# Optimization experiments

Measured on AMD Instinct MI355X. Metric: run time of the kernel, lower is better.

## Reference

```python
import jax, jax.numpy as jnp
import numpy as np

EMBED_DIM = 1024
NUM_HEADS = 16
HEAD_DIM = EMBED_DIM // NUM_HEADS
SCALE = 1.0 / np.sqrt(HEAD_DIM).astype(np.float32)


def setup_inputs() -> dict:
    key = jax.random.key(0)
    ks = jax.random.split(key, 9)
    B, T, C = 2, 2048, EMBED_DIM
    s = 1.0 / np.sqrt(C).astype(np.float32)  # torch Linear init scale (approx, uniform bound)
    return {
        "x_q": jax.random.normal(ks[0], (B, T, C), dtype=jnp.float32),
        "attn_mask": jnp.zeros((T, T), dtype=jnp.float32),
        "Wq": jax.random.uniform(ks[1], (C, C), jnp.float32, -s, s),
        "bq": jax.random.uniform(ks[2], (C,), jnp.float32, -s, s),
        "Wk": jax.random.uniform(ks[3], (C, C), jnp.float32, -s, s),
        "bk": jax.random.uniform(ks[4], (C,), jnp.float32, -s, s),
        "Wv": jax.random.uniform(ks[5], (C, C), jnp.float32, -s, s),
        "bv": jax.random.uniform(ks[6], (C,), jnp.float32, -s, s),
        "Wo": jax.random.uniform(ks[7], (C, C), jnp.float32, -s, s),
        "bo": jax.random.uniform(ks[8], (C,), jnp.float32, -s, s),
    }


def reference(x_q, attn_mask, Wq, bq, Wk, bk, Wv, bv, Wo, bo):
    B, Tq, C = x_q.shape
    # self-attention: x_kv = x_q
    q = (x_q @ Wq.T + bq).reshape(B, Tq, NUM_HEADS, HEAD_DIM)
    k = (x_q @ Wk.T + bk).reshape(B, Tq, NUM_HEADS, HEAD_DIM)
    v = (x_q @ Wv.T + bv).reshape(B, Tq, NUM_HEADS, HEAD_DIM)
    # (B, H, Tq, Tk)
    scores = jnp.einsum('bqhd,bkhd->bhqk', q, k) * SCALE
    scores = scores + attn_mask[None, None, :, :]  # 2D additive mask path
    attn = jax.nn.softmax(scores, axis=-1)  # dropout p=0.0 -> identity
    out = jnp.einsum('bhqk,bkhd->bqhd', attn, v).reshape(B, Tq, C)
    out = out @ Wo.T + bo
    return out
```

## Files before the change

kernel.cpp:

```cpp
#include <hip/hip_runtime.h>
#include <hip/hip_bf16.h>
#include <stdint.h>

typedef _Float16 f16x8_t __attribute__((ext_vector_type(8)));
typedef _Float16 f16x4_t __attribute__((ext_vector_type(4)));
typedef float    f32x4_t __attribute__((ext_vector_type(4)));

#define T_SEQ 2048
#define NH    16
#define HD    64
#define CDIM  1024
#define NTOK  4096
#define QSCALE 0.18033688011112042f
#define LOG2E  1.4426950408889634f

__device__ __forceinline__ void async_ld16(void* lds, const void* g) {
    __builtin_amdgcn_global_load_lds(
        (const __attribute__((address_space(1))) uint32_t*)g,
        (__attribute__((address_space(3))) uint32_t*)lds, 16, 0, 0);
}

__global__ __launch_bounds__(256)
void prep_all(const float* __restrict__ x, const float* __restrict__ Wq,
              const float* __restrict__ Wk, const float* __restrict__ Wv,
              const float* __restrict__ Wo, const float* __restrict__ mask,
              _Float16* __restrict__ xh, _Float16* __restrict__ Wqkvh,
              _Float16* __restrict__ Woh, int* __restrict__ flag)
{
    const int XQ = NTOK * CDIM / 4;
    const int WQ = CDIM * CDIM / 4;
    int i = blockIdx.x * 256 + threadIdx.x;
    if (i < XQ + 4 * WQ) {
        const float* s; _Float16* d; int off;
        if (i < XQ) { s = x; d = xh; off = i; }
        else {
            int j = i - XQ; int w = j >> 18; off = j & (WQ - 1);
            s = (w == 0) ? Wq : (w == 1) ? Wk : (w == 2) ? Wv : Wo;
            d = (w == 3) ? Woh : Wqkvh + (size_t)w * CDIM * CDIM;
        }
        float4 v = ((const float4*)s)[off];
        f16x4_t h = {(_Float16)v.x, (_Float16)v.y, (_Float16)v.z, (_Float16)v.w};
        ((f16x4_t*)d)[off] = h;
    } else {
        int off = i - (XQ + 4 * WQ);
        float4 v = ((const float4*)mask)[off];
        if (v.x != 0.f || v.y != 0.f || v.z != 0.f || v.w != 0.f) atomicOr(flag, 1);
    }
}

template<int MODE>
__global__ __launch_bounds__(256)
void gemm_f16(const _Float16* __restrict__ Ag, const _Float16* __restrict__ Bg,
              const float* __restrict__ b0, const float* __restrict__ b1,
              const float* __restrict__ b2,
              _Float16* __restrict__ Qo, _Float16* __restrict__ Ko,
              _Float16* __restrict__ Vto, float* __restrict__ Fo)
{
    __shared__ _Float16 sA[2][128 * 32];
    __shared__ _Float16 sB[2][128 * 32];
    const int K = CDIM;
    const int NBX = (MODE == 0) ? 24 : 8;
    const int NWG = NBX * 32;
    const int tid  = threadIdx.x;
    const int lane = tid & 63, wv = tid >> 6;
    const int wr = wv >> 1, wc = wv & 1;
    const int bid = blockIdx.x;
    const int swz = (bid & 7) * (NWG / 8) + (bid >> 3);
    const int rowA0 = (swz % NBX) * 128;
    const int rowB0 = (swz / NBX) * 128;
    const int srow = lane >> 2;
    const int scol = (lane & 3) * 8;
    const int fr = lane & 15, fg = lane >> 4;
    f32x4_t acc[4][4] = {};

#define STAGE(buf, kk) do {                                                     \
        _Pragma("unroll")                                                       \
        for (int i_ = 0; i_ < 2; ++i_) {                                        \
            const int eoff = i_ * 2048 + wv * 512;                              \
            const int r_ = i_ * 64 + wv * 16 + srow;                            \
            async_ld16(&sA[buf][eoff], Ag + (size_t)(rowA0 + r_) * K + (kk) + scol); \
            async_ld16(&sB[buf][eoff], Bg + (size_t)(rowB0 + r_) * K + (kk) + scol); \
        } } while (0)

    STAGE(0, 0);
    for (int k0 = 0; k0 < K; k0 += 32) {
        const int cur = (k0 >> 5) & 1;
        __syncthreads();
        if (k0 + 32 < K) STAGE(cur ^ 1, k0 + 32);
        f16x8_t a[4], b[4];
#pragma unroll
        for (int mi = 0; mi < 4; ++mi)
            a[mi] = *(const f16x8_t*)&sA[cur][(wr * 64 + mi * 16 + fr) * 32 + fg * 8];
#pragma unroll
        for (int ni = 0; ni < 4; ++ni)
            b[ni] = *(const f16x8_t*)&sB[cur][(wc * 64 + ni * 16 + fr) * 32 + fg * 8];
#pragma unroll
        for (int mi = 0; mi < 4; ++mi)
#pragma unroll
            for (int ni = 0; ni < 4; ++ni)
                acc[mi][ni] = __builtin_amdgcn_mfma_f32_16x16x32_f16(a[mi], b[ni], acc[mi][ni], 0, 0, 0);
    }
#undef STAGE

    if (MODE == 0) {
        const int which = rowA0 >> 10;
        const float* bp = (which == 0) ? b0 : ((which == 1) ? b1 : b2);
#pragma unroll
        for (int mi = 0; mi < 4; ++mi) {
            const int cc = (rowA0 & 1023) + wr * 64 + mi * 16 + fg * 4;
            const float4 bv = *(const float4*)&bp[cc];
            const int h = cc >> 6, d0 = cc & 63;
#pragma unroll
            for (int ni = 0; ni < 4; ++ni) {
                const int tok = rowB0 + wc * 64 + ni * 16 + fr;
                const int bh = (tok >> 11) * NH + h, tt = tok & (T_SEQ - 1);
                const float v0 = acc[mi][ni][0] + bv.x, v1 = acc[mi][ni][1] + bv.y;
                const float v2 = acc[mi][ni][2] + bv.z, v3 = acc[mi][ni][3] + bv.w;
                if (which == 0) {
                    f16x4_t hq = {(_Float16)(v0 * QSCALE), (_Float16)(v1 * QSCALE),
                                  (_Float16)(v2 * QSCALE), (_Float16)(v3 * QSCALE)};
                    *(f16x4_t*)&Qo[((size_t)bh * T_SEQ + tt) * HD + d0] = hq;
                } else if (which == 1) {
                    f16x4_t hk = {(_Float16)v0, (_Float16)v1, (_Float16)v2, (_Float16)v3};
                    *(f16x4_t*)&Ko[((size_t)bh * 32 + (tt >> 6)) * 4096 +
                                   (d0 >> 3) * 512 + (tt & 63) * 8 + (d0 & 7)] = hk;
                } else {
                    const size_t vb_ = ((size_t)bh * 32 + (tt >> 6)) * 4096 +
                                       (size_t)((tt >> 3) & 7) * 512 + (tt & 7);
                    Vto[vb_ + (d0 + 0) * 8] = (_Float16)v0;
                    Vto[vb_ + (d0 + 1) * 8] = (_Float16)v1;
                    Vto[vb_ + (d0 + 2) * 8] = (_Float16)v2;
                    Vto[vb_ + (d0 + 3) * 8] = (_Float16)v3;
                }
            }
        }
    } else {
#pragma unroll
        for (int mi = 0; mi < 4; ++mi) {
            const int cc = rowA0 + wr * 64 + mi * 16 + fg * 4;
            const float4 bv = *(const float4*)&b0[cc];
#pragma unroll
            for (int ni = 0; ni < 4; ++ni) {
                const int tok = rowB0 + wc * 64 + ni * 16 + fr;
                float4 ov = {acc[mi][ni][0] + bv.x, acc[mi][ni][1] + bv.y,
                             acc[mi][ni][2] + bv.z, acc[mi][ni][3] + bv.w};
                *(float4*)&Fo[(size_t)tok * CDIM + cc] = ov;
            }
        }
    }
}

__global__ __launch_bounds__(256, 4)
void attn_f16(const _Float16* __restrict__ Q, const _Float16* __restrict__ Kc,
              const _Float16* __restrict__ Vc, const float* __restrict__ mask,
              const int* __restrict__ mflag, _Float16* __restrict__ AO)
{
    __shared__ __align__(16) _Float16 sK[2][4096];
    __shared__ __align__(16) _Float16 sV[2][4096];
    __shared__ __align__(16) _Float16 Ps[4][1024];

    const int tid = threadIdx.x;
    const int lane = tid & 63, wv = tid >> 6;
    const int fr = lane & 15, fg = lane >> 4;
    const int bid = blockIdx.x;
    const int swz = (bid & 7) * 128 + (bid >> 3);
    const int qx = swz & 31, bh = swz >> 5;
    const int b = bh >> 4, h = bh & (NH - 1);
    const int q0 = qx * 64 + wv * 16;
    const _Float16* Qb  = Q  + (size_t)bh * T_SEQ * HD;
    const _Float16* Kbh = Kc + (size_t)bh * (T_SEQ * HD);
    const _Float16* Vbh = Vc + (size_t)bh * (T_SEQ * HD);
    const int soff = wv * 512 + lane * 8;

    f16x8_t qf[2];
#pragma unroll
    for (int dc = 0; dc < 2; ++dc)
        qf[dc] = *(const f16x8_t*)&Qb[(size_t)(q0 + fr) * HD + dc * 32 + fg * 8];

    const f16x8_t ones = {(_Float16)1.f, (_Float16)1.f, (_Float16)1.f, (_Float16)1.f,
                          (_Float16)1.f, (_Float16)1.f, (_Float16)1.f, (_Float16)1.f};
    f32x4_t o[4] = {};
    f32x4_t lacc = {};
    float m_run = -1e30f;
    const int mf = mflag[0];

    async_ld16(&sK[0][soff],        Kbh + soff);
    async_ld16(&sK[0][2048 + soff], Kbh + 2048 + soff);
    async_ld16(&sV[0][soff],        Vbh + soff);
    async_ld16(&sV[0][2048 + soff], Vbh + 2048 + soff);

    for (int t = 0; t < T_SEQ / 64; ++t) {
        const int cur = t & 1;
        __syncthreads();
        if (t + 1 < T_SEQ / 64) {
            const int nb = cur ^ 1, goff = (t + 1) * 4096;
            async_ld16(&sK[nb][soff],        Kbh + goff + soff);
            async_ld16(&sK[nb][2048 + soff], Kbh + goff + 2048 + soff);
            async_ld16(&sV[nb][soff],        Vbh + goff + soff);
            async_ld16(&sV[nb][2048 + soff], Vbh + goff + 2048 + soff);
        }

        f32x4_t s[4];
        __builtin_amdgcn_s_setprio(1);
#pragma unroll
        for (int kt = 0; kt < 4; ++kt) {
            f16x8_t kf0 = *(const f16x8_t*)&sK[cur][fg * 512       + (kt * 16 + fr) * 8];
            f16x8_t kf1 = *(const f16x8_t*)&sK[cur][(4 + fg) * 512 + (kt * 16 + fr) * 8];
            f32x4_t z = {};
            z     = __builtin_amdgcn_mfma_f32_16x16x32_f16(kf0, qf[0], z, 0, 0, 0);
            s[kt] = __builtin_amdgcn_mfma_f32_16x16x32_f16(kf1, qf[1], z, 0, 0, 0);
        }
        __builtin_amdgcn_s_setprio(0);

        f16x8_t vb[2][4];
#pragma unroll
        for (int kt2 = 0; kt2 < 2; ++kt2)
#pragma unroll
            for (int df = 0; df < 4; ++df)
                vb[kt2][df] = *(const f16x8_t*)&sV[cur][(kt2 * 4 + fg) * 512 + (df * 16 + fr) * 8];

        if (mf) {
            const float* mrow = mask + (size_t)(q0 + fr) * T_SEQ + t * 64;
#pragma unroll
            for (int kt = 0; kt < 4; ++kt)
#pragma unroll
                for (int r = 0; r < 4; ++r)
                    s[kt][r] += mrow[kt * 16 + fg * 4 + r] * LOG2E;
        }

        const float t0 = fmaxf(fmaxf(s[0][0], s[0][1]), s[0][2]);
        const float t1 = fmaxf(fmaxf(s[0][3], s[1][0]), s[1][1]);
        const float t2 = fmaxf(fmaxf(s[1][2], s[1][3]), s[2][0]);
        const float t3 = fmaxf(fmaxf(s[2][1], s[2][2]), s[2][3]);
        const float t4 = fmaxf(fmaxf(s[3][0], s[3][1]), s[3][2]);
        float tmax = fmaxf(fmaxf(fmaxf(t0, t1), fmaxf(t2, t3)), fmaxf(t4, s[3][3]));
        tmax = fmaxf(tmax, __shfl_xor(tmax, 16, 64));
        tmax = fmaxf(tmax, __shfl_xor(tmax, 32, 64));

        if (!__all(tmax <= m_run + 8.0f)) {
            const float mnew = fmaxf(m_run, tmax);
            const float sc = __builtin_amdgcn_exp2f(m_run - mnew);
            m_run = mnew;
            float scq[4];
#pragma unroll
            for (int r = 0; r < 4; ++r)
                scq[r] = __shfl(sc, fg * 4 + r, 64);
#pragma unroll
            for (int r = 0; r < 4; ++r) {
                lacc[r] *= scq[r];
#pragma unroll
                for (int df = 0; df < 4; ++df)
                    o[df][r] *= scq[r];
            }
        }

#pragma unroll
        for (int kt = 0; kt < 4; ++kt) {
            f16x4_t hp;
#pragma unroll
            for (int r = 0; r < 4; ++r)
                hp[r] = (_Float16)__builtin_amdgcn_exp2f(s[kt][r] - m_run);
            *(f16x4_t*)&Ps[wv][(kt * 2 + (fg >> 1)) * 128 + fr * 8 + (fg & 1) * 4] = hp;
        }

        asm volatile("s_waitcnt lgkmcnt(0)" ::: "memory");
        __builtin_amdgcn_sched_barrier(0);

        __builtin_amdgcn_s_setprio(1);
#pragma unroll
        for (int kt2 = 0; kt2 < 2; ++kt2) {
            f16x8_t pa = *(const f16x8_t*)&Ps[wv][(kt2 * 4 + fg) * 128 + fr * 8];
#pragma unroll
            for (int df = 0; df < 4; ++df)
                o[df] = __builtin_amdgcn_mfma_f32_16x16x32_f16(pa, vb[kt2][df], o[df], 0, 0, 0);
            lacc = __builtin_amdgcn_mfma_f32_16x16x32_f16(pa, ones, lacc, 0, 0, 0);
        }
        __builtin_amdgcn_s_setprio(0);
    }

#pragma unroll
    for (int r = 0; r < 4; ++r) {
        const float inv = 1.f / lacc[r];
        const size_t row = (size_t)(b * T_SEQ + q0 + fg * 4 + r);
#pragma unroll
        for (int df = 0; df < 4; ++df)
            AO[row * CDIM + h * HD + df * 16 + fr] = (_Float16)(o[df][r] * inv);
    }
}

extern "C" void kernel_launch(void* const* d_in, const int* in_sizes, int n_in,
                              void* d_out, int out_size, void* d_ws, size_t ws_size,
                              hipStream_t stream) {
    const float* x    = (const float*)d_in[0];
    const float* mask = (const float*)d_in[1];
    const float* Wq   = (const float*)d_in[2];
    const float* bq   = (const float*)d_in[3];
    const float* Wk   = (const float*)d_in[4];
    const float* bk   = (const float*)d_in[5];
    const float* Wv   = (const float*)d_in[6];
    const float* bv   = (const float*)d_in[7];
    const float* Wo   = (const float*)d_in[8];
    const float* bo   = (const float*)d_in[9];
    float* out = (float*)d_out;

    char* ws = (char*)d_ws;
    _Float16* xh    = (_Float16*)(ws);
    _Float16* Wqkvh = (_Float16*)(ws + (8u  << 20));
    _Float16* Woh   = (_Float16*)(ws + (14u << 20));
    _Float16* Qp    = (_Float16*)(ws + (16u << 20));
    _Float16* Kc    = (_Float16*)(ws + (24u << 20));
    _Float16* Vc    = (_Float16*)(ws + (32u << 20));
    int* mflag      = (int*)(ws + (40u << 20));
    _Float16* AO    = xh;

    hipMemsetAsync(mflag, 0, 4, stream);
    prep_all<<<12288, 256, 0, stream>>>(x, Wq, Wk, Wv, Wo, mask, xh, Wqkvh, Woh, mflag);
    gemm_f16<0><<<768, 256, 0, stream>>>(Wqkvh, xh, bq, bk, bv, Qp, Kc, Vc, nullptr);
    attn_f16<<<1024, 256, 0, stream>>>(Qp, Kc, Vc, mask, mflag, AO);
    gemm_f16<1><<<256, 256, 0, stream>>>(Woh, AO, bo, nullptr, nullptr,
                                         nullptr, nullptr, nullptr, out);
}
```

Measured before the change: 135.2 us.

## Switch attention to 32x32 MFMA tiles with register-resident P via permlane swap

Rewrites the attention kernel so each wave handles 32 query rows using 32x32x16 MFMA instructions, with 128 queries per block and half as many blocks. The softmax probabilities stay in registers and are rearranged with v_permlane32_swap instead of a round trip through LDS. The row sum is now accumulated with scalar adds plus a shuffle instead of an extra MFMA against a ones vector. This removes LDS traffic and the wait that came with it, at the cost of higher register pressure (launch bounds lowered to 2 blocks per CU) and fewer blocks in flight.

Result: faster. 131.0 us (-3.1%).

```diff
diff --git a/kernel.cpp b/kernel.cpp
--- a/kernel.cpp
+++ b/kernel.cpp
@@ -5,6 +5,7 @@
 typedef _Float16 f16x8_t __attribute__((ext_vector_type(8)));
 typedef _Float16 f16x4_t __attribute__((ext_vector_type(4)));
 typedef float    f32x4_t __attribute__((ext_vector_type(4)));
+typedef float    f32x16_t __attribute__((ext_vector_type(16)));
 
 #define T_SEQ 2048
 #define NH    16
@@ -150,38 +151,34 @@
     }
 }
 
-__global__ __launch_bounds__(256, 4)
+__global__ __launch_bounds__(256, 2)
 void attn_f16(const _Float16* __restrict__ Q, const _Float16* __restrict__ Kc,
               const _Float16* __restrict__ Vc, const float* __restrict__ mask,
               const int* __restrict__ mflag, _Float16* __restrict__ AO)
 {
     __shared__ __align__(16) _Float16 sK[2][4096];
     __shared__ __align__(16) _Float16 sV[2][4096];
-    __shared__ __align__(16) _Float16 Ps[4][1024];
 
     const int tid = threadIdx.x;
     const int lane = tid & 63, wv = tid >> 6;
-    const int fr = lane & 15, fg = lane >> 4;
+    const int ln = lane & 31, hi = lane >> 5;
     const int bid = blockIdx.x;
-    const int swz = (bid & 7) * 128 + (bid >> 3);
-    const int qx = swz & 31, bh = swz >> 5;
+    const int swz = (bid & 7) * 64 + (bid >> 3);
+    const int qx = swz & 15, bh = swz >> 4;
     const int b = bh >> 4, h = bh & (NH - 1);
-    const int q0 = qx * 64 + wv * 16;
+    const int q0 = qx * 128 + wv * 32;
     const _Float16* Qb  = Q  + (size_t)bh * T_SEQ * HD;
     const _Float16* Kbh = Kc + (size_t)bh * (T_SEQ * HD);
     const _Float16* Vbh = Vc + (size_t)bh * (T_SEQ * HD);
-    const int soff = wv * 512 + lane * 8;
-
-    f16x8_t qf[2];
-#pragma unroll
-    for (int dc = 0; dc < 2; ++dc)
-        qf[dc] = *(const f16x8_t*)&Qb[(size_t)(q0 + fr) * HD + dc * 32 + fg * 8];
-
-    const f16x8_t ones = {(_Float16)1.f, (_Float16)1.f, (_Float16)1.f, (_Float16)1.f,
-                          (_Float16)1.f, (_Float16)1.f, (_Float16)1.f, (_Float16)1.f};
-    f32x4_t o[4] = {};
-    f32x4_t lacc = {};
-    float m_run = -1e30f;
+    const int soff = tid * 8;
+
+    f16x8_t qf[4];
+#pragma unroll
+    for (int dc = 0; dc < 4; ++dc)
+        qf[dc] = *(const f16x8_t*)&Qb[(size_t)(q0 + ln) * HD + dc * 16 + hi * 8];
+
+    f32x16_t o0 = {}, o1 = {};
+    float m_run = -1e30f, l_run = 0.f;
     const int mf = mflag[0];
 
     async_ld16(&sK[0][soff],        Kbh + soff);
@@ -200,91 +197,107 @@
             async_ld16(&sV[nb][2048 + soff], Vbh + goff + 2048 + soff);
         }
 
-        f32x4_t s[4];
+        f32x16_t s0 = {}, s1 = {};
         __builtin_amdgcn_s_setprio(1);
 #pragma unroll
-        for (int kt = 0; kt < 4; ++kt) {
-            f16x8_t kf0 = *(const f16x8_t*)&sK[cur][fg * 512       + (kt * 16 + fr) * 8];
-            f16x8_t kf1 = *(const f16x8_t*)&sK[cur][(4 + fg) * 512 + (kt * 16 + fr) * 8];
-            f32x4_t z = {};
-            z     = __builtin_amdgcn_mfma_f32_16x16x32_f16(kf0, qf[0], z, 0, 0, 0);
-            s[kt] = __builtin_amdgcn_mfma_f32_16x16x32_f16(kf1, qf[1], z, 0, 0, 0);
+        for (int dc = 0; dc < 4; ++dc) {
+            f16x8_t kf0 = *(const f16x8_t*)&sK[cur][(2 * dc + hi) * 512 + ln * 8];
+            f16x8_t kf1 = *(const f16x8_t*)&sK[cur][(2 * dc + hi) * 512 + (32 + ln) * 8];
+            s0 = __builtin_amdgcn_mfma_f32_32x32x16_f16(kf0, qf[dc], s0, 0, 0, 0);
+            s1 = __builtin_amdgcn_mfma_f32_32x32x16_f16(kf1, qf[dc], s1, 0, 0, 0);
         }
         __builtin_amdgcn_s_setprio(0);
 
-        f16x8_t vb[2][4];
-#pragma unroll
-        for (int kt2 = 0; kt2 < 2; ++kt2)
-#pragma unroll
-            for (int df = 0; df < 4; ++df)
-                vb[kt2][df] = *(const f16x8_t*)&sV[cur][(kt2 * 4 + fg) * 512 + (df * 16 + fr) * 8];
-
         if (mf) {
-            const float* mrow = mask + (size_t)(q0 + fr) * T_SEQ + t * 64;
-#pragma unroll
-            for (int kt = 0; kt < 4; ++kt)
-#pragma unroll
-                for (int r = 0; r < 4; ++r)
-                    s[kt][r] += mrow[kt * 16 + fg * 4 + r] * LOG2E;
-        }
-
-        const float t0 = fmaxf(fmaxf(s[0][0], s[0][1]), s[0][2]);
-        const float t1 = fmaxf(fmaxf(s[0][3], s[1][0]), s[1][1]);
-        const float t2 = fmaxf(fmaxf(s[1][2], s[1][3]), s[2][0]);
-        const float t3 = fmaxf(fmaxf(s[2][1], s[2][2]), s[2][3]);
-        const float t4 = fmaxf(fmaxf(s[3][0], s[3][1]), s[3][2]);
-        float tmax = fmaxf(fmaxf(fmaxf(t0, t1), fmaxf(t2, t3)), fmaxf(t4, s[3][3]));
-        tmax = fmaxf(tmax, __shfl_xor(tmax, 16, 64));
-        tmax = fmaxf(tmax, __shfl_xor(tmax, 32, 64));
+            const float* mrow = mask + (size_t)(q0 + ln) * T_SEQ + t * 64;
+#pragma unroll
+            for (int r2 = 0; r2 < 16; ++r2) {
+                const int row = (r2 & 3) + 8 * (r2 >> 2) + 4 * hi;
+                s0[r2] += mrow[row] * LOG2E;
+                s1[r2] += mrow[32 + row] * LOG2E;
+            }
+        }
+
+        float mt[8];
+#pragma unroll
+        for (int i = 0; i < 8; ++i)
+            mt[i] = fmaxf(fmaxf(s0[2 * i], s0[2 * i + 1]), fmaxf(s1[2 * i], s1[2 * i + 1]));
+#pragma unroll
+        for (int st = 4; st > 0; st >>= 1)
+#pragma unroll
+            for (int i = 0; i < st; ++i) mt[i] = fmaxf(mt[i], mt[i + st]);
+        float tmax = fmaxf(mt[0], __shfl_xor(mt[0], 32, 64));
 
         if (!__all(tmax <= m_run + 8.0f)) {
             const float mnew = fmaxf(m_run, tmax);
             const float sc = __builtin_amdgcn_exp2f(m_run - mnew);
             m_run = mnew;
-            float scq[4];
-#pragma unroll
-            for (int r = 0; r < 4; ++r)
-                scq[r] = __shfl(sc, fg * 4 + r, 64);
-#pragma unroll
-            for (int r = 0; r < 4; ++r) {
-                lacc[r] *= scq[r];
-#pragma unroll
-                for (int df = 0; df < 4; ++df)
-                    o[df][r] *= scq[r];
-            }
-        }
-
-#pragma unroll
-        for (int kt = 0; kt < 4; ++kt) {
-            f16x4_t hp;
-#pragma unroll
-            for (int r = 0; r < 4; ++r)
-                hp[r] = (_Float16)__builtin_amdgcn_exp2f(s[kt][r] - m_run);
-            *(f16x4_t*)&Ps[wv][(kt * 2 + (fg >> 1)) * 128 + fr * 8 + (fg & 1) * 4] = hp;
-        }
-
-        asm volatile("s_waitcnt lgkmcnt(0)" ::: "memory");
-        __builtin_amdgcn_sched_barrier(0);
+            l_run *= sc;
+#pragma unroll
+            for (int r2 = 0; r2 < 16; ++r2) {
+                const int row = (r2 & 3) + 8 * (r2 >> 2) + 4 * hi;
+                const float scr = __shfl(sc, row, 64);
+                o0[r2] *= scr;
+                o1[r2] *= scr;
+            }
+        }
+
+#pragma unroll
+        for (int r2 = 0; r2 < 16; ++r2) {
+            s0[r2] = __builtin_amdgcn_exp2f(s0[r2] - m_run);
+            s1[r2] = __builtin_amdgcn_exp2f(s1[r2] - m_run);
+        }
+        float sm[8];
+#pragma unroll
+        for (int i = 0; i < 8; ++i)
+            sm[i] = (s0[2 * i] + s0[2 * i + 1]) + (s1[2 * i] + s1[2 * i + 1]);
+#pragma unroll
+        for (int st = 4; st > 0; st >>= 1)
+#pragma unroll
+            for (int i = 0; i < st; ++i) sm[i] += sm[i + st];
+        l_run += sm[0] + __shfl_xor(sm[0], 32, 64);
+
+        f16x8_t pa[4];
+#pragma unroll
+        for (int g = 0; g < 2; ++g) {
+            const f32x16_t& sg = g ? s1 : s0;
+            uint32_t W[8];
+#pragma unroll
+            for (int t2 = 0; t2 < 8; ++t2) {
+                auto pk = __builtin_amdgcn_cvt_pkrtz(sg[2 * t2], sg[2 * t2 + 1]);
+                W[t2] = __builtin_bit_cast(uint32_t, pk);
+            }
+#pragma unroll
+            for (int c2 = 0; c2 < 2; ++c2) {
+                uint32_t a0 = W[4 * c2 + 0], a1 = W[4 * c2 + 1];
+                uint32_t a2 = W[4 * c2 + 2], a3 = W[4 * c2 + 3];
+                asm("v_permlane32_swap_b32 %0, %1" : "+v"(a0), "+v"(a2));
+                asm("v_permlane32_swap_b32 %0, %1" : "+v"(a1), "+v"(a3));
+                union { uint32_t w[4]; f16x8_t v; } u;
+                u.w[0] = a0; u.w[1] = a1; u.w[2] = a2; u.w[3] = a3;
+                pa[g * 2 + c2] = u.v;
+            }
+        }
 
         __builtin_amdgcn_s_setprio(1);
 #pragma unroll
-        for (int kt2 = 0; kt2 < 2; ++kt2) {
-            f16x8_t pa = *(const f16x8_t*)&Ps[wv][(kt2 * 4 + fg) * 128 + fr * 8];
-#pragma unroll
-            for (int df = 0; df < 4; ++df)
-                o[df] = __builtin_amdgcn_mfma_f32_16x16x32_f16(pa, vb[kt2][df], o[df], 0, 0, 0);
-            lacc = __builtin_amdgcn_mfma_f32_16x16x32_f16(pa, ones, lacc, 0, 0, 0);
+        for (int c = 0; c < 4; ++c) {
+            f16x8_t vb0 = *(const f16x8_t*)&sV[cur][(2 * c + hi) * 512 + ln * 8];
+            f16x8_t vb1 = *(const f16x8_t*)&sV[cur][(2 * c + hi) * 512 + (32 + ln) * 8];
+            o0 = __builtin_amdgcn_mfma_f32_32x32x16_f16(pa[c], vb0, o0, 0, 0, 0);
+            o1 = __builtin_amdgcn_mfma_f32_32x32x16_f16(pa[c], vb1, o1, 0, 0, 0);
         }
         __builtin_amdgcn_s_setprio(0);
     }
 
-#pragma unroll
-    for (int r = 0; r < 4; ++r) {
-        const float inv = 1.f / lacc[r];
-        const size_t row = (size_t)(b * T_SEQ + q0 + fg * 4 + r);
-#pragma unroll
-        for (int df = 0; df < 4; ++df)
-            AO[row * CDIM + h * HD + df * 16 + fr] = (_Float16)(o[df][r] * inv);
+    const float linv = 1.f / l_run;
+#pragma unroll
+    for (int r2 = 0; r2 < 16; ++r2) {
+        const int row = (r2 & 3) + 8 * (r2 >> 2) + 4 * hi;
+        const float inv = __shfl(linv, row, 64);
+        const size_t base = (size_t)(b * T_SEQ + q0 + row) * CDIM + h * HD;
+        AO[base + ln]      = (_Float16)(o0[r2] * inv);
+        AO[base + 32 + ln] = (_Float16)(o1[r2] * inv);
     }
 }
 
@@ -316,7 +329,7 @@
     hipMemsetAsync(mflag, 0, 4, stream);
     prep_all<<<12288, 256, 0, stream>>>(x, Wq, Wk, Wv, Wo, mask, xh, Wqkvh, Woh, mflag);
     gemm_f16<0><<<768, 256, 0, stream>>>(Wqkvh, xh, bq, bk, bv, Qp, Kc, Vc, nullptr);
-    attn_f16<<<1024, 256, 0, stream>>>(Qp, Kc, Vc, mask, mflag, AO);
+    attn_f16<<<512, 256, 0, stream>>>(Qp, Kc, Vc, mask, mflag, AO);
     gemm_f16<1><<<256, 256, 0, stream>>>(Woh, AO, bo, nullptr, nullptr,
                                          nullptr, nullptr, nullptr, out);
 }
```
